# Kernel tuning notes

Measured on AMD Instinct MI355X. Metric: run time of the kernel, lower is better.

The kernel has to match this reference:

```python
import jax, jax.numpy as jnp
import numpy as np

D_MODEL = 512
N_HEADS = 8
DEPTH = D_MODEL // N_HEADS
NEG_INF = -1000000000.0


def setup_inputs() -> dict:
    key = jax.random.key(0)
    ks = jax.random.split(key, 12)
    B, S = 4, 2048
    scale = 0.02
    return {
        "Q": jax.random.normal(ks[0], (B, S, D_MODEL), jnp.float32),
        "K": jax.random.normal(ks[1], (B, S, D_MODEL), jnp.float32),
        "V": jax.random.normal(ks[2], (B, S, D_MODEL), jnp.float32),
        "mask": jax.random.randint(ks[3], (B, S, S), 0, 2, jnp.int32),
        "Wq": jax.random.normal(ks[4], (D_MODEL, D_MODEL), jnp.float32) * scale,
        "bq": jnp.zeros((D_MODEL,), jnp.float32),
        "Wk": jax.random.normal(ks[5], (D_MODEL, D_MODEL), jnp.float32) * scale,
        "bk": jnp.zeros((D_MODEL,), jnp.float32),
        "Wv": jax.random.normal(ks[6], (D_MODEL, D_MODEL), jnp.float32) * scale,
        "bv": jnp.zeros((D_MODEL,), jnp.float32),
        "Wo": jax.random.normal(ks[7], (D_MODEL, D_MODEL), jnp.float32) * scale,
        "bo": jnp.zeros((D_MODEL,), jnp.float32),
    }


def _split_heads(x, B):
    # [B, S, d_model] -> [B, H, S, depth]
    S = x.shape[1]
    return x.reshape(B, S, N_HEADS, DEPTH).transpose(0, 2, 1, 3)


def reference(Q, K, V, mask, Wq, bq, Wk, bk, Wv, bv, Wo, bo):
    B, S, _ = Q.shape
    q = _split_heads(Q @ Wq + bq, B)  # [B,H,S,d]
    k = _split_heads(K @ Wk + bk, B)
    v = _split_heads(V @ Wv + bv, B)
    scores = jnp.einsum("bhqd,bhkd->bhqk", q, k) / jnp.sqrt(
        jnp.asarray(DEPTH, jnp.float32))
    m = mask[:, None, :, :]  # broadcast over heads: [B,1,S,S]
    scores = jnp.where(m == 0, jnp.asarray(NEG_INF, scores.dtype), scores)
    attn = jax.nn.softmax(scores, axis=-1)
    ctx = jnp.einsum("bhqk,bhkd->bhqd", attn, v)
    ctx = ctx.transpose(0, 2, 1, 3).reshape(B, S, D_MODEL)
    return ctx @ Wo + bo
```

## Files before the change

kernel.cpp:

```cpp
#include <hip/hip_runtime.h>
#include <hip/hip_bf16.h>
#include <stdint.h>

typedef unsigned short u16;
typedef unsigned int u32;
typedef unsigned long long u64;
using bf16x8 = __attribute__((ext_vector_type(8))) __bf16;
using f32x4  = __attribute__((ext_vector_type(4))) float;
using f32x16 = __attribute__((ext_vector_type(16))) float;

static constexpr int B_ = 4, H_ = 8, S_ = 2048, D_ = 64, DM_ = 512;
#define QSCALE 0.1803368801111601f

__device__ __forceinline__ u16 f2b(float f) {
  u32 u = __float_as_uint(f);
  u = (u + 0x7FFFu + ((u >> 16) & 1u)) >> 16;
  return (u16)u;
}

__device__ __forceinline__ u32 cvtpk_bf16(float a, float b) {
  u32 r;
  asm("v_cvt_pk_bf16_f32 %0, %1, %2" : "=v"(r) : "v"(a), "v"(b));
  return r;
}
__device__ __forceinline__ void plswap(u32& a, u32& b) {
  asm("v_permlane32_swap_b32 %0, %1" : "+v"(a), "+v"(b));
}
__device__ __forceinline__ void gload16(const void* g, void* lds) {
  __builtin_amdgcn_global_load_lds(
      (const __attribute__((address_space(1))) u32*)g,
      (__attribute__((address_space(3))) u32*)lds, 16, 0, 0);
}
#if __has_builtin(__builtin_amdgcn_exp2f)
__device__ __forceinline__ float exp2fast(float x) { return __builtin_amdgcn_exp2f(x); }
#else
__device__ __forceinline__ float exp2fast(float x) {
  float r;
  asm("v_exp_f32 %0, %1" : "=v"(r) : "v"(x));
  return r;
}
#endif
__device__ __forceinline__ float selmask(float ex, u64 pred) {
  float r;
  asm("v_cndmask_b32 %0, 0, %1, %2" : "=v"(r) : "v"(ex), "s"(pred));
  return r;
}

__global__ __launch_bounds__(256) void cast3_kernel(
    const float* __restrict__ Q, const float* __restrict__ K, const float* __restrict__ V,
    u16* __restrict__ Qb, u16* __restrict__ Kb, u16* __restrict__ Vb) {
  const int z = blockIdx.z;
  const float* src = z == 0 ? Q : z == 1 ? K : V;
  u16* dst        = z == 0 ? Qb : z == 1 ? Kb : Vb;
  const int i = blockIdx.x * 256 + threadIdx.x;
  float4 v = reinterpret_cast<const float4*>(src)[i];
  uint2 o;
  o.x = cvtpk_bf16(v.x, v.y);
  o.y = cvtpk_bf16(v.z, v.w);
  reinterpret_cast<uint2*>(dst)[i] = o;
}

__global__ __launch_bounds__(256) void prep_w_kernel(
    const float* __restrict__ Wq, const float* __restrict__ Wk,
    const float* __restrict__ Wv, const float* __restrict__ Wo,
    u16* __restrict__ Wtq, u16* __restrict__ Wtk, u16* __restrict__ Wtv, u16* __restrict__ Wto) {
  __shared__ float tile[32][33];
  const int z = blockIdx.z;
  const float* W = z == 0 ? Wq : z == 1 ? Wk : z == 2 ? Wv : Wo;
  u16* Wt       = z == 0 ? Wtq : z == 1 ? Wtk : z == 2 ? Wtv : Wto;
  const int k0 = blockIdx.x * 32, n0 = blockIdx.y * 32;
  const int t = threadIdx.x;
  {
    const int kl = t >> 3, nl4 = (t & 7) * 4;
    float4 v = *(const float4*)(W + (size_t)(k0 + kl) * DM_ + n0 + nl4);
    tile[kl][nl4 + 0] = v.x; tile[kl][nl4 + 1] = v.y;
    tile[kl][nl4 + 2] = v.z; tile[kl][nl4 + 3] = v.w;
  }
  __syncthreads();
  {
    const int nl = t >> 3, kl4 = (t & 7) * 4;
    ushort4 o;
    o.x = f2b(tile[kl4 + 0][nl]); o.y = f2b(tile[kl4 + 1][nl]);
    o.z = f2b(tile[kl4 + 2][nl]); o.w = f2b(tile[kl4 + 3][nl]);
    *(ushort4*)(Wt + (size_t)(n0 + nl) * DM_ + k0 + kl4) = o;
  }
}

__global__ __launch_bounds__(256) void pack_mask_kernel(const int* __restrict__ mask,
                                                        u64* __restrict__ wmask) {
  __shared__ int mt[4][32][65];
  const int t = threadIdx.x, lane = t & 63, w = t >> 6;
  const int kt = blockIdx.x * 4 + w, qg = blockIdx.y, b = blockIdx.z;
  const int q0 = qg * 32;
  const int* src = mask + ((size_t)b * S_ + q0) * S_ + kt * 64 + lane;
#pragma unroll 8
  for (int i = 0; i < 32; ++i) mt[w][i][lane] = src[(size_t)i * S_];
  u64* dst = wmask + (((size_t)(b * 64 + qg) * 32 + kt) * 32);
  const int hi4 = (lane >> 5) * 4;
#pragma unroll
  for (int idx = 0; idx < 32; ++idx) {
    const int ksub = idx >> 4, r = idx & 15;
    const int key = ksub * 32 + (r & 3) + 8 * (r >> 2) + hi4;
    u64 bal = __ballot(mt[w][lane & 31][key] != 0);
    if (lane == 0) dst[idx] = bal;
  }
}

__global__ __launch_bounds__(256) void gemm_qkv_kernel(
    const u16* __restrict__ Qb, const u16* __restrict__ Kb, const u16* __restrict__ Vb,
    const u16* __restrict__ Wtq, const u16* __restrict__ Wtk, const u16* __restrict__ Wtv,
    const float* __restrict__ bq, const float* __restrict__ bk, const float* __restrict__ bv,
    u16* __restrict__ qp, u16* __restrict__ kp, u16* __restrict__ vp) {
  __shared__ __align__(16) u16 As[128 * 32];
  __shared__ __align__(16) u16 Bs[128 * 32];
  const int z = blockIdx.z;
  const u16* A      = z == 0 ? Qb : z == 1 ? Kb : Vb;
  const u16* Bt     = z == 0 ? Wtq : z == 1 ? Wtk : Wtv;
  const float* bias = z == 0 ? bq : z == 1 ? bk : bv;
  u16* outp         = z == 0 ? qp : z == 1 ? kp : vp;
  const float scale = z == 0 ? QSCALE : 1.0f;

  const int t = threadIdx.x;
  const int lane = t & 63, wid = t >> 6;
  const int wr = wid >> 1, wc = wid & 1;
  const int l15 = lane & 15, l4 = lane >> 4;
  const int cn = blockIdx.x * 128, rm = blockIdx.y * 128;

  const int srow = wid * 16 + (lane >> 2), scol = (lane & 3) * 8;
  const u16* asrc = A + (size_t)(rm + srow) * DM_ + scol;
  const u16* bsrc = Bt + (size_t)(cn + srow) * DM_ + scol;
  char* adst = (char*)As + wid * 1024;
  char* bdst = (char*)Bs + wid * 1024;

  f32x4 acc[4][4] = {};

  for (int k0 = 0; k0 < DM_; k0 += 32) {
    __syncthreads();
    gload16(asrc + k0, adst);
    gload16(asrc + (size_t)64 * DM_ + k0, adst + 4096);
    gload16(bsrc + k0, bdst);
    gload16(bsrc + (size_t)64 * DM_ + k0, bdst + 4096);
    __syncthreads();
    bf16x8 af[4], bfr[4];
#pragma unroll
    for (int m = 0; m < 4; ++m)
      af[m] = *(const bf16x8*)((const char*)As + (wr * 64 + m * 16 + l15) * 64 + l4 * 16);
#pragma unroll
    for (int n = 0; n < 4; ++n)
      bfr[n] = *(const bf16x8*)((const char*)Bs + (wc * 64 + n * 16 + l15) * 64 + l4 * 16);
#pragma unroll
    for (int m = 0; m < 4; ++m)
#pragma unroll
      for (int n = 0; n < 4; ++n)
        acc[m][n] = __builtin_amdgcn_mfma_f32_16x16x32_bf16(af[m], bfr[n], acc[m][n], 0, 0, 0);
  }

#pragma unroll
  for (int m = 0; m < 4; ++m)
#pragma unroll
    for (int n = 0; n < 4; ++n) {
      int col = cn + wc * 64 + n * 16 + l15;
      float bv_ = bias[col];
#pragma unroll
      for (int r = 0; r < 4; ++r) {
        int row = rm + wr * 64 + m * 16 + l4 * 4 + r;
        float v = (acc[m][n][r] + bv_) * scale;
        int b = row >> 11, s = row & 2047;
        int h = col >> 6, d = col & 63;
        if (z < 2)
          outp[(((size_t)(b * H_ + h)) * S_ + s) * D_ + d] = f2b(v);
        else
          outp[(((size_t)(b * H_ + h)) * D_ + d) * S_ + s] = f2b(v);
      }
    }
}

__global__ __launch_bounds__(256) void gemm_out_kernel(
    const u16* __restrict__ A, const u16* __restrict__ Bt,
    const float* __restrict__ bias, float* __restrict__ outp) {
  __shared__ __align__(16) u16 As[64 * 32];
  __shared__ __align__(16) u16 Bs[128 * 32];
  const int t = threadIdx.x;
  const int lane = t & 63, w = t >> 6;
  const int l15 = lane & 15, l4 = lane >> 4;
  const int cn = blockIdx.x * 128, rm = blockIdx.y * 64;

  const int srow = w * 16 + (lane >> 2), scol = (lane & 3) * 8;
  const u16* asrc = A + (size_t)(rm + srow) * DM_ + scol;
  const u16* bsrc = Bt + (size_t)(cn + srow) * DM_ + scol;
  char* adst = (char*)As + w * 1024;
  char* bdst = (char*)Bs + w * 1024;

  f32x4 acc[4][2] = {};

  for (int k0 = 0; k0 < DM_; k0 += 32) {
    __syncthreads();
    gload16(asrc + k0, adst);
    gload16(bsrc + k0, bdst);
    gload16(bsrc + (size_t)64 * DM_ + k0, bdst + 4096);
    __syncthreads();
    bf16x8 af[4], bfr[2];
#pragma unroll
    for (int m = 0; m < 4; ++m)
      af[m] = *(const bf16x8*)((const char*)As + (m * 16 + l15) * 64 + l4 * 16);
#pragma unroll
    for (int n = 0; n < 2; ++n)
      bfr[n] = *(const bf16x8*)((const char*)Bs + (w * 32 + n * 16 + l15) * 64 + l4 * 16);
#pragma unroll
    for (int m = 0; m < 4; ++m)
#pragma unroll
      for (int n = 0; n < 2; ++n)
        acc[m][n] = __builtin_amdgcn_mfma_f32_16x16x32_bf16(af[m], bfr[n], acc[m][n], 0, 0, 0);
  }

#pragma unroll
  for (int m = 0; m < 4; ++m)
#pragma unroll
    for (int n = 0; n < 2; ++n) {
      int col = cn + w * 32 + n * 16 + l15;
      float bv_ = bias[col];
#pragma unroll
      for (int r = 0; r < 4; ++r) {
        int row = rm + m * 16 + l4 * 4 + r;
        outp[(size_t)row * DM_ + col] = acc[m][n][r] + bv_;
      }
    }
}

__global__ __launch_bounds__(256, 4) void attn_kernel(
    const u16* __restrict__ qp, const u16* __restrict__ kp, const u16* __restrict__ vp,
    const u64* __restrict__ wmask, u16* __restrict__ ctx) {
  __shared__ __align__(16) char smem[32768];
  const int t = threadIdx.x, lane = t & 63, w = t >> 6;
  const int l31 = lane & 31, hi = lane >> 5;
  const int ksub = w & 1, qsub = w >> 1;
  const int wu = __builtin_amdgcn_readfirstlane(w);
  const int wgid = blockIdx.x;
  const int h = wgid & 7, idx = wgid >> 3;
  const int b = idx >> 5, qt = idx & 31;
  const size_t head  = ((size_t)(b * H_ + h)) * S_ * D_;
  const size_t headT = ((size_t)(b * H_ + h)) * D_ * S_;
  const int q0 = qt * 64 + qsub * 32;
  const int q  = q0 + l31;

  bf16x8 qf[4];
  {
    const u16* qrow = qp + head + (size_t)q * D_;
#pragma unroll
    for (int ks = 0; ks < 4; ++ks) qf[ks] = *(const bf16x8*)(qrow + ks * 16 + hi * 8);
  }

  const u64* wm = wmask + (((size_t)(b * 64 + qt * 2 + (wu >> 1)) * 32) * 32) + (wu & 1) * 16;

  const int kxor = (l31 & 7) << 4;
  const int krbase = (ksub * 32 + l31) * 128;
  const int rbase0 = l31 * 128, rbase1 = (32 + l31) * 128;
  int colx[4];
#pragma unroll
  for (int s = 0; s < 4; ++s) colx[s] = ((s * 32 + hi * 16) ^ kxor);
  int vcolx[2];
#pragma unroll
  for (int s = 0; s < 2; ++s) vcolx[s] = ((ksub * 64 + s * 32 + hi * 16) ^ kxor);

  const int srow = lane >> 3;
  const int scol = ((lane & 7) ^ srow) << 3;
  const int c0 = w, c1 = w + 4;
  const u16* ksrc0 = kp + head + (size_t)(c0 * 8 + srow) * D_ + scol;
  const u16* ksrc1 = kp + head + (size_t)(c1 * 8 + srow) * D_ + scol;
  const u16* vsrc0 = vp + headT + (size_t)(c0 * 8 + srow) * S_ + scol;
  const u16* vsrc1 = vp + headT + (size_t)(c1 * 8 + srow) * S_ + scol;

  f32x16 accO0, accO1, lacc, FZ;
#pragma unroll
  for (int i = 0; i < 16; ++i) { accO0[i] = 0.f; accO1[i] = 0.f; lacc[i] = 0.f; FZ[i] = 0.f; }
  union { u32 wds[4]; bf16x8 v; } ones;
#pragma unroll
  for (int i = 0; i < 4; ++i) ones.wds[i] = 0x3F803F80u;

  auto stage = [&](int bufi, int kt) {
    char* kb = smem + bufi * 8192;
    char* vb = smem + 16384 + bufi * 8192;
    gload16(ksrc0 + (size_t)kt * 4096, kb + c0 * 1024);
    gload16(ksrc1 + (size_t)kt * 4096, kb + c1 * 1024);
    gload16(vsrc0 + kt * 64, vb + c0 * 1024);
    gload16(vsrc1 + kt * 64, vb + c1 * 1024);
  };

  stage(0, 0);
  u64 mskr[16];
#pragma unroll
  for (int r = 0; r < 16; ++r) mskr[r] = wm[r];
  __syncthreads();
  int buf = 0;

  for (int kt = 0; kt < S_ / 64; ++kt) {
    if (kt < S_ / 64 - 1) stage(buf ^ 1, kt + 1);

    const char* kb = smem + buf * 8192;
    const char* vb = smem + 16384 + buf * 8192;

    f32x16 s;
    {
      bf16x8 kf[4];
#pragma unroll
      for (int ks = 0; ks < 4; ++ks) kf[ks] = *(const bf16x8*)(kb + krbase + colx[ks]);
      __builtin_amdgcn_s_setprio(1);
      s = __builtin_amdgcn_mfma_f32_32x32x16_bf16(kf[0], qf[0], FZ, 0, 0, 0);
#pragma unroll
      for (int ks = 1; ks < 4; ++ks)
        s = __builtin_amdgcn_mfma_f32_32x32x16_bf16(kf[ks], qf[ks], s, 0, 0, 0);
      __builtin_amdgcn_s_setprio(0);
    }

    float e[16];
#pragma unroll
    for (int r = 0; r < 16; ++r) e[r] = selmask(exp2fast(s[r]), mskr[r]);

    {
      u32 pw[8];
#pragma unroll
      for (int j = 0; j < 8; ++j)
        pw[j] = cvtpk_bf16(e[2 * j], e[2 * j + 1]);
      plswap(pw[0], pw[2]); plswap(pw[1], pw[3]);
      plswap(pw[4], pw[6]); plswap(pw[5], pw[7]);
      __builtin_amdgcn_s_setprio(1);
#pragma unroll
      for (int s2 = 0; s2 < 2; ++s2) {
        union { u32 wds[4]; bf16x8 v; } pa;
        pa.wds[0] = pw[s2 * 4 + 0]; pa.wds[1] = pw[s2 * 4 + 1];
        pa.wds[2] = pw[s2 * 4 + 2]; pa.wds[3] = pw[s2 * 4 + 3];
        bf16x8 vf0 = *(const bf16x8*)(vb + rbase0 + vcolx[s2]);
        accO0 = __builtin_amdgcn_mfma_f32_32x32x16_bf16(pa.v, vf0, accO0, 0, 0, 0);
        bf16x8 vf1 = *(const bf16x8*)(vb + rbase1 + vcolx[s2]);
        accO1 = __builtin_amdgcn_mfma_f32_32x32x16_bf16(pa.v, vf1, accO1, 0, 0, 0);
        lacc = __builtin_amdgcn_mfma_f32_32x32x16_bf16(pa.v, ones.v, lacc, 0, 0, 0);
      }
      __builtin_amdgcn_s_setprio(0);
    }

    if (kt < S_ / 64 - 1) {
      const u64* wmk = wm + (kt + 1) * 32;
#pragma unroll
      for (int r = 0; r < 16; ++r) mskr[r] = wmk[r];
    }
    __syncthreads();
    buf ^= 1;
  }

  float (*Ol)[32][64] = (float (*)[32][64])smem;
  float (*La)[32] = (float (*)[32])(smem + 16384);
  if (ksub == 1) {
#pragma unroll
    for (int r = 0; r < 16; ++r) {
      const int qr = (r & 3) + 8 * (r >> 2) + 4 * hi;
      Ol[qsub][qr][l31]      = accO0[r];
      Ol[qsub][qr][32 + l31] = accO1[r];
      if (l31 == 0) La[qsub][qr] = lacc[r];
    }
  }
  __syncthreads();
  if (ksub == 0) {
    const int colA = h * 64 + l31, colB = h * 64 + 32 + l31;
#pragma unroll
    for (int r = 0; r < 16; ++r) {
      const int qr = (r & 3) + 8 * (r >> 2) + 4 * hi;
      const int row = q0 + qr;
      const float inv = 1.0f / (lacc[r] + La[qsub][qr]);
      u16* o = ctx + ((size_t)(b * S_) + row) * DM_;
      o[colA] = f2b((accO0[r] + Ol[qsub][qr][l31])      * inv);
      o[colB] = f2b((accO1[r] + Ol[qsub][qr][32 + l31]) * inv);
    }
  }
}

extern "C" void kernel_launch(void* const* d_in, const int* in_sizes, int n_in,
                              void* d_out, int out_size, void* d_ws, size_t ws_size,
                              hipStream_t stream) {
  const float* Q  = (const float*)d_in[0];
  const float* K  = (const float*)d_in[1];
  const float* V  = (const float*)d_in[2];
  const int* mask = (const int*)d_in[3];
  const float* Wq = (const float*)d_in[4];
  const float* bq = (const float*)d_in[5];
  const float* Wk = (const float*)d_in[6];
  const float* bk = (const float*)d_in[7];
  const float* Wv = (const float*)d_in[8];
  const float* bv = (const float*)d_in[9];
  const float* Wo = (const float*)d_in[10];
  const float* bo = (const float*)d_in[11];

  char* ws = (char*)d_ws;
  size_t off = 0;
  auto alloc = [&](size_t bytes) -> void* {
    void* p = ws + off;
    off += (bytes + 255) & ~(size_t)255;
    return p;
  };
  const size_t act_b = (size_t)B_ * S_ * DM_ * 2;
  u16* Wtq = (u16*)alloc((size_t)DM_ * DM_ * 2);
  u16* Wtk = (u16*)alloc((size_t)DM_ * DM_ * 2);
  u16* Wtv = (u16*)alloc((size_t)DM_ * DM_ * 2);
  u16* Wto = (u16*)alloc((size_t)DM_ * DM_ * 2);
  u64* wmask = (u64*)alloc((size_t)B_ * 64 * 32 * 32 * 8);
  u16* Qb  = (u16*)alloc(act_b);
  u16* Kb  = (u16*)alloc(act_b);
  u16* Vb  = (u16*)alloc(act_b);
  u16* qp  = (u16*)alloc(act_b);
  u16* kp  = (u16*)alloc(act_b);
  u16* vp  = (u16*)alloc(act_b);
  u16* ctx = (u16*)alloc(act_b);

  prep_w_kernel<<<dim3(16, 16, 4), 256, 0, stream>>>(Wq, Wk, Wv, Wo, Wtq, Wtk, Wtv, Wto);
  pack_mask_kernel<<<dim3(8, 64, 4), 256, 0, stream>>>(mask, wmask);
  cast3_kernel<<<dim3((B_ * S_ * DM_ / 4) / 256, 1, 3), 256, 0, stream>>>(Q, K, V, Qb, Kb, Vb);

  gemm_qkv_kernel<<<dim3(4, 64, 3), 256, 0, stream>>>(
      Qb, Kb, Vb, Wtq, Wtk, Wtv, bq, bk, bv, qp, kp, vp);

  attn_kernel<<<dim3(1024), 256, 0, stream>>>(qp, kp, vp, wmask, ctx);

  gemm_out_kernel<<<dim3(4, 128), 256, 0, stream>>>(ctx, Wto, bo, (float*)d_out);
}
```

Baseline: 130.6 us.

## Fuse fp32-to-bf16 cast into QKV GEMM and triple-buffer attention K/V staging

Removes the separate cast kernel: the QKV GEMM now loads fp32 activations directly into LDS and converts them to bf16 when building MFMA fragments. This saves a full write and re-read of three bf16 activation tensors and one launch, at the price of twice the LDS traffic for the A operand. The attention kernel also moves from double to triple buffering of K/V tiles with explicit vmcnt waits and a raw barrier instead of __syncthreads. That keeps two tiles in flight, but LDS grows to 48KB and occupancy drops from 4 to 3 blocks.

```diff
diff --git a/kernel.cpp b/kernel.cpp
--- a/kernel.cpp
+++ b/kernel.cpp
@@ -44,20 +44,6 @@
   float r;
   asm("v_cndmask_b32 %0, 0, %1, %2" : "=v"(r) : "v"(ex), "s"(pred));
   return r;
-}
-
-__global__ __launch_bounds__(256) void cast3_kernel(
-    const float* __restrict__ Q, const float* __restrict__ K, const float* __restrict__ V,
-    u16* __restrict__ Qb, u16* __restrict__ Kb, u16* __restrict__ Vb) {
-  const int z = blockIdx.z;
-  const float* src = z == 0 ? Q : z == 1 ? K : V;
-  u16* dst        = z == 0 ? Qb : z == 1 ? Kb : Vb;
-  const int i = blockIdx.x * 256 + threadIdx.x;
-  float4 v = reinterpret_cast<const float4*>(src)[i];
-  uint2 o;
-  o.x = cvtpk_bf16(v.x, v.y);
-  o.y = cvtpk_bf16(v.z, v.w);
-  reinterpret_cast<uint2*>(dst)[i] = o;
 }
 
 __global__ __launch_bounds__(256) void prep_w_kernel(
@@ -107,14 +93,14 @@
 }
 
 __global__ __launch_bounds__(256) void gemm_qkv_kernel(
-    const u16* __restrict__ Qb, const u16* __restrict__ Kb, const u16* __restrict__ Vb,
+    const float* __restrict__ Qf, const float* __restrict__ Kf, const float* __restrict__ Vf,
     const u16* __restrict__ Wtq, const u16* __restrict__ Wtk, const u16* __restrict__ Wtv,
     const float* __restrict__ bq, const float* __restrict__ bk, const float* __restrict__ bv,
     u16* __restrict__ qp, u16* __restrict__ kp, u16* __restrict__ vp) {
-  __shared__ __align__(16) u16 As[128 * 32];
-  __shared__ __align__(16) u16 Bs[128 * 32];
+  __shared__ __align__(16) float As[128 * 32];
+  __shared__ __align__(16) u16  Bs[128 * 32];
   const int z = blockIdx.z;
-  const u16* A      = z == 0 ? Qb : z == 1 ? Kb : Vb;
+  const float* A    = z == 0 ? Qf : z == 1 ? Kf : Vf;
   const u16* Bt     = z == 0 ? Wtq : z == 1 ? Wtk : Wtv;
   const float* bias = z == 0 ? bq : z == 1 ? bk : bv;
   u16* outp         = z == 0 ? qp : z == 1 ? kp : vp;
@@ -126,25 +112,33 @@
   const int l15 = lane & 15, l4 = lane >> 4;
   const int cn = blockIdx.x * 128, rm = blockIdx.y * 128;
 
-  const int srow = wid * 16 + (lane >> 2), scol = (lane & 3) * 8;
-  const u16* asrc = A + (size_t)(rm + srow) * DM_ + scol;
-  const u16* bsrc = Bt + (size_t)(cn + srow) * DM_ + scol;
+  const int arow = t >> 3, acol = (t & 7) * 4;
+  const float* asrc = A + (size_t)(rm + arow) * DM_ + acol;
   char* adst = (char*)As + wid * 1024;
+  const int brow = t >> 2, bcol = (t & 3) * 8;
+  const u16* bsrc = Bt + (size_t)(cn + brow) * DM_ + bcol;
   char* bdst = (char*)Bs + wid * 1024;
 
   f32x4 acc[4][4] = {};
 
   for (int k0 = 0; k0 < DM_; k0 += 32) {
     __syncthreads();
-    gload16(asrc + k0, adst);
-    gload16(asrc + (size_t)64 * DM_ + k0, adst + 4096);
+#pragma unroll
+    for (int i = 0; i < 4; ++i)
+      gload16(asrc + (size_t)(i * 32) * DM_ + k0, adst + i * 4096);
     gload16(bsrc + k0, bdst);
     gload16(bsrc + (size_t)64 * DM_ + k0, bdst + 4096);
     __syncthreads();
     bf16x8 af[4], bfr[4];
 #pragma unroll
-    for (int m = 0; m < 4; ++m)
-      af[m] = *(const bf16x8*)((const char*)As + (wr * 64 + m * 16 + l15) * 64 + l4 * 16);
+    for (int m = 0; m < 4; ++m) {
+      const float* ap = As + (wr * 64 + m * 16 + l15) * 32 + l4 * 8;
+      float4 x = *(const float4*)ap, y = *(const float4*)(ap + 4);
+      union { u32 wds[4]; bf16x8 v; } c;
+      c.wds[0] = cvtpk_bf16(x.x, x.y); c.wds[1] = cvtpk_bf16(x.z, x.w);
+      c.wds[2] = cvtpk_bf16(y.x, y.y); c.wds[3] = cvtpk_bf16(y.z, y.w);
+      af[m] = c.v;
+    }
 #pragma unroll
     for (int n = 0; n < 4; ++n)
       bfr[n] = *(const bf16x8*)((const char*)Bs + (wc * 64 + n * 16 + l15) * 64 + l4 * 16);
@@ -227,10 +221,10 @@
     }
 }
 
-__global__ __launch_bounds__(256, 4) void attn_kernel(
+__global__ __launch_bounds__(256, 3) void attn_kernel(
     const u16* __restrict__ qp, const u16* __restrict__ kp, const u16* __restrict__ vp,
     const u64* __restrict__ wmask, u16* __restrict__ ctx) {
-  __shared__ __align__(16) char smem[32768];
+  __shared__ __align__(16) char smem[49152];
   const int t = threadIdx.x, lane = t & 63, w = t >> 6;
   const int l31 = lane & 31, hi = lane >> 5;
   const int ksub = w & 1, qsub = w >> 1;
@@ -278,26 +272,30 @@
   for (int i = 0; i < 4; ++i) ones.wds[i] = 0x3F803F80u;
 
   auto stage = [&](int bufi, int kt) {
-    char* kb = smem + bufi * 8192;
-    char* vb = smem + 16384 + bufi * 8192;
+    char* kb = smem + bufi * 16384;
+    char* vb = kb + 8192;
     gload16(ksrc0 + (size_t)kt * 4096, kb + c0 * 1024);
     gload16(ksrc1 + (size_t)kt * 4096, kb + c1 * 1024);
     gload16(vsrc0 + kt * 64, vb + c0 * 1024);
     gload16(vsrc1 + kt * 64, vb + c1 * 1024);
   };
 
+  constexpr int NT = S_ / 64;
   stage(0, 0);
+  stage(1, 1);
   u64 mskr[16];
 #pragma unroll
   for (int r = 0; r < 16; ++r) mskr[r] = wm[r];
-  __syncthreads();
-  int buf = 0;
-
-  for (int kt = 0; kt < S_ / 64; ++kt) {
-    if (kt < S_ / 64 - 1) stage(buf ^ 1, kt + 1);
-
-    const char* kb = smem + buf * 8192;
-    const char* vb = smem + 16384 + buf * 8192;
+  asm volatile("s_waitcnt vmcnt(4)" ::: "memory");
+  __builtin_amdgcn_s_barrier();
+  asm volatile("" ::: "memory");
+
+  for (int kt = 0; kt < NT; ++kt) {
+    const int cur = kt % 3;
+    if (kt < NT - 2) stage((kt + 2) % 3, kt + 2);
+
+    const char* kb = smem + cur * 16384;
+    const char* vb = kb + 8192;
 
     f32x16 s;
     {
@@ -338,13 +336,21 @@
       __builtin_amdgcn_s_setprio(0);
     }
 
-    if (kt < S_ / 64 - 1) {
+    if (kt < NT - 1) {
       const u64* wmk = wm + (kt + 1) * 32;
 #pragma unroll
       for (int r = 0; r < 16; ++r) mskr[r] = wmk[r];
     }
-    __syncthreads();
-    buf ^= 1;
+
+    if (kt < NT - 1) {
+      if (kt < NT - 2) {
+        asm volatile("s_waitcnt vmcnt(4)" ::: "memory");
+      } else {
+        asm volatile("s_waitcnt vmcnt(0)" ::: "memory");
+      }
+      __builtin_amdgcn_s_barrier();
+      asm volatile("" ::: "memory");
+    }
   }
 
   float (*Ol)[32][64] = (float (*)[32][64])smem;
@@ -402,9 +408,6 @@
   u16* Wtv = (u16*)alloc((size_t)DM_ * DM_ * 2);
   u16* Wto = (u16*)alloc((size_t)DM_ * DM_ * 2);
   u64* wmask = (u64*)alloc((size_t)B_ * 64 * 32 * 32 * 8);
-  u16* Qb  = (u16*)alloc(act_b);
-  u16* Kb  = (u16*)alloc(act_b);
-  u16* Vb  = (u16*)alloc(act_b);
   u16* qp  = (u16*)alloc(act_b);
   u16* kp  = (u16*)alloc(act_b);
   u16* vp  = (u16*)alloc(act_b);
@@ -412,10 +415,9 @@
 
   prep_w_kernel<<<dim3(16, 16, 4), 256, 0, stream>>>(Wq, Wk, Wv, Wo, Wtq, Wtk, Wtv, Wto);
   pack_mask_kernel<<<dim3(8, 64, 4), 256, 0, stream>>>(mask, wmask);
-  cast3_kernel<<<dim3((B_ * S_ * DM_ / 4) / 256, 1, 3), 256, 0, stream>>>(Q, K, V, Qb, Kb, Vb);
 
   gemm_qkv_kernel<<<dim3(4, 64, 3), 256, 0, stream>>>(
-      Qb, Kb, Vb, Wtq, Wtk, Wtv, bq, bk, bv, qp, kp, vp);
+      Q, K, V, Wtq, Wtk, Wtv, bq, bk, bv, qp, kp, vp);
 
   attn_kernel<<<dim3(1024), 256, 0, stream>>>(qp, kp, vp, wmask, ctx);
 
```

New measurement: 132.0 us. No clear change (+1.1%).
